# Kernel tuning notes

Hardware: AMD Instinct MI355X
Metric: run time of the kernel (lower is better)

The kernel has to match this reference:

```python
import jax, jax.numpy as jnp
import numpy as np

N = 50000          # nodes
E = 800000         # edges (before self-loops)
F_IN = 128         # num_features
HID = 16           # hidden_dim (per head)
HEADS = 4
NG = 128           # number of graphs in batch
NC = 10            # num_classes
LAYERS = 3
NEG_SLOPE = 0.2    # PyG GATConv default
EPS = 1e-16


def setup_inputs() -> dict:
    key = jax.random.key(0)
    ks = jax.random.split(key, 4 + 4 * LAYERS + 2)
    inp = {}
    inp["x"] = jax.random.normal(ks[0], (N, F_IN), jnp.float32)
    inp["edge_index"] = jax.random.randint(ks[1], (2, E), 0, N, dtype=jnp.int32)
    inp["batch"] = jnp.sort(jax.random.randint(ks[2], (N,), 0, NG, dtype=jnp.int32))
    in_dims = [F_IN] + [HID * HEADS] * (LAYERS - 1)
    for i in range(LAYERS):
        kb = 3 + 4 * i
        s = 1.0 / np.sqrt(in_dims[i])
        inp[f"W{i}"] = jax.random.normal(ks[kb], (in_dims[i], HEADS * HID), jnp.float32) * s
        inp[f"b{i}"] = jnp.zeros((HEADS * HID,), jnp.float32)
        inp[f"as{i}"] = jax.random.normal(ks[kb + 1], (HEADS, HID), jnp.float32) * 0.1
        inp[f"ad{i}"] = jax.random.normal(ks[kb + 2], (HEADS, HID), jnp.float32) * 0.1
    inp["Wr"] = jax.random.normal(ks[3 + 4 * LAYERS], (HEADS * HID, NC), jnp.float32) * (1.0 / np.sqrt(HEADS * HID))
    inp["br"] = jnp.zeros((NC,), jnp.float32)
    return inp


def _gat_layer(x, src, dst, W, b, att_src, att_dst):
    n = x.shape[0]
    h = (x @ W).reshape(n, HEADS, HID)                # [N,H,D]
    a_src = jnp.einsum('nhd,hd->nh', h, att_src)      # [N,H]
    a_dst = jnp.einsum('nhd,hd->nh', h, att_dst)
    logits = jax.nn.leaky_relu(a_src[src] + a_dst[dst], NEG_SLOPE)  # [E,H]
    # segment softmax over destination node
    m = jax.ops.segment_max(logits, dst, num_segments=n)
    e = jnp.exp(logits - m[dst])
    s = jax.ops.segment_sum(e, dst, num_segments=n)
    alpha = e / (s[dst] + EPS)                        # [E,H]
    msg = h[src] * alpha[:, :, None]                  # [E,H,D]
    out = jax.ops.segment_sum(msg, dst, num_segments=n)
    return out.reshape(n, HEADS * HID) + b


def reference(x, edge_index, batch,
              W0, b0, as0, ad0,
              W1, b1, as1, ad1,
              W2, b2, as2, ad2,
              Wr, br):
    # add self loops (PyG GATConv default add_self_loops=True)
    loop = jnp.arange(N, dtype=edge_index.dtype)
    src = jnp.concatenate([edge_index[0], loop])
    dst = jnp.concatenate([edge_index[1], loop])
    params = [(W0, b0, as0, ad0), (W1, b1, as1, ad1), (W2, b2, as2, ad2)]
    h = x
    for (W, b, a_s, a_d) in params:
        h = _gat_layer(h, src, dst, W, b, a_s, a_d)
        h = jax.nn.silu(h)
        # dropout p=0.0 (eval): identity
    pooled = jax.ops.segment_sum(h, batch, num_segments=NG)   # [NG, H*D]
    logits = jax.nn.relu(pooled @ Wr + br)                    # make_mlp ends with ReLU
    return jax.nn.log_softmax(logits, axis=1)
```

## Files before the change

kernel.cpp:

```cpp
#include <hip/hip_runtime.h>
#include <hip/hip_fp16.h>
#include <cstdint>
#include <cstddef>

#define HEADS 4
#define HID 16
#define HD 64
#define NCLS 10
#define NGRAPH 128
#define NEG_SLOPE 0.2f
#define SM_EPS 1e-16f
#define SLOTS 64

static inline size_t alignup(size_t x) { return (x + 255) & ~size_t(255); }

__device__ __forceinline__ unsigned short f2h(float f) {
    __half h = __float2half(f);
    return *reinterpret_cast<unsigned short*>(&h);
}

__global__ void scatter_kernel(const int* __restrict__ srcA, const int* __restrict__ dstA,
                               int E, int npg, int* __restrict__ cursor,
                               unsigned short* __restrict__ csr_src) {
    int g = blockIdx.x & 7;
    int c = blockIdx.x >> 3;
    int nchunks = gridDim.x >> 3;
    int chunk = (E + nchunks - 1) / nchunks;
    int start = c * chunk;
    int end = min(E, start + chunk);
    int lo = g * npg, hi = lo + npg;
    for (int e = start + threadIdx.x; e < end; e += blockDim.x) {
        int d = dstA[e];
        if (d >= lo && d < hi) {
            int pos = atomicAdd(&cursor[d], 1);
            if (pos < SLOTS) csr_src[(size_t)d * SLOTS + pos] = (unsigned short)srcA[e];
        }
    }
}


__global__ __launch_bounds__(256) void gemm_attn_kernel(
        const float* __restrict__ in, const float* __restrict__ Wp,
        const float* __restrict__ as_, const float* __restrict__ ad_,
        unsigned short* __restrict__ hb, float* __restrict__ asrc,
        float* __restrict__ adst, int N, int K) {
    __shared__ __align__(16) float xs[64][68];
    __shared__ __align__(16) float Ws[64][64];
    __shared__ float avl[HD], adl[HD];
    int tid = threadIdx.x, lane = tid & 63, wave = tid >> 6;
    int cg = lane & 15;
    int c0 = cg * 4;
    int r0 = wave * 16 + (lane >> 4) * 4;
    if (tid < HD) { avl[tid] = as_[tid]; adl[tid] = ad_[tid]; }

    int base = blockIdx.x * 64;
    float acc[4][4];
#pragma unroll
    for (int i = 0; i < 4; i++)
#pragma unroll
        for (int j = 0; j < 4; j++) acc[i][j] = 0.f;

    for (int kh = 0; kh < K; kh += 64) {
        __syncthreads();
        for (int i = tid; i < 1024; i += 256) {
            int r = i >> 4, c = (i & 15) * 4;
            float4 v = make_float4(0.f, 0.f, 0.f, 0.f);
            if (base + r < N) v = *(const float4*)(in + (size_t)(base + r) * K + kh + c);
            *(float4*)&xs[r][c] = v;
        }
        for (int i = tid; i < 1024; i += 256) {
            int r = i >> 4, c = (i & 15) * 4;
            *(float4*)&Ws[r][c] = *(const float4*)(Wp + (size_t)(kh + r) * HD + c);
        }
        __syncthreads();

#pragma unroll 8
        for (int k = 0; k < 64; k += 4) {
            float4 wv[4], xv[4];
#pragma unroll
            for (int j = 0; j < 4; j++) wv[j] = *(const float4*)&Ws[k + j][c0];
#pragma unroll
            for (int i = 0; i < 4; i++) xv[i] = *(const float4*)&xs[r0 + i][k];
#pragma unroll
            for (int i = 0; i < 4; i++) {
                acc[i][0] += xv[i].x * wv[0].x + xv[i].y * wv[1].x + xv[i].z * wv[2].x + xv[i].w * wv[3].x;
                acc[i][1] += xv[i].x * wv[0].y + xv[i].y * wv[1].y + xv[i].z * wv[2].y + xv[i].w * wv[3].y;
                acc[i][2] += xv[i].x * wv[0].z + xv[i].y * wv[1].z + xv[i].z * wv[2].z + xv[i].w * wv[3].z;
                acc[i][3] += xv[i].x * wv[0].w + xv[i].y * wv[1].w + xv[i].z * wv[2].w + xv[i].w * wv[3].w;
            }
        }
    }

    int head = cg >> 2;
#pragma unroll
    for (int i = 0; i < 4; i++) {
        int node = base + r0 + i;
        float s = acc[i][0] * avl[c0] + acc[i][1] * avl[c0 + 1] +
                  acc[i][2] * avl[c0 + 2] + acc[i][3] * avl[c0 + 3];
        float d = acc[i][0] * adl[c0] + acc[i][1] * adl[c0 + 1] +
                  acc[i][2] * adl[c0 + 2] + acc[i][3] * adl[c0 + 3];
        s += __shfl_xor(s, 1); s += __shfl_xor(s, 2);
        d += __shfl_xor(d, 1); d += __shfl_xor(d, 2);
        if (node < N) {
            ushort4 pk;
            pk.x = f2h(acc[i][0]); pk.y = f2h(acc[i][1]);
            pk.z = f2h(acc[i][2]); pk.w = f2h(acc[i][3]);
            *(ushort4*)&hb[(size_t)node * HD + c0] = pk;
            if ((cg & 3) == 0) {
                asrc[node * HEADS + head] = s;
                adst[node * HEADS + head] = d;
            }
        }
    }
}

__global__ void gat_gather_kernel(const int* __restrict__ deg,
                                  const unsigned short* __restrict__ csr_src,
                                  int N, const unsigned short* __restrict__ hb,
                                  const float* __restrict__ asrc, const float* __restrict__ adst,
                                  const float* __restrict__ bias, float* __restrict__ out) {
    int wid = (int)((blockIdx.x * (long long)blockDim.x + threadIdx.x) >> 6);
    if (wid >= N) return;
    int lane = threadIdx.x & 63;
    int hh = lane & 3;
    int eg = lane >> 2;
    int e2 = lane >> 5;
    int cp = lane & 31;
    int headc = cp >> 3;

    int beg = wid * SLOTS;
    int cnt = min(deg[wid], SLOTS);
    int end = beg + cnt;

    float4 as4 = *(const float4*)&asrc[wid * 4];
    float4 ad4 = *(const float4*)&adst[wid * 4];
    float l0 = as4.x + ad4.x; l0 = l0 > 0.f ? l0 : NEG_SLOPE * l0;
    float l1 = as4.y + ad4.y; l1 = l1 > 0.f ? l1 : NEG_SLOPE * l1;
    float l2 = as4.z + ad4.z; l2 = l2 > 0.f ? l2 : NEG_SLOPE * l2;
    float l3 = as4.w + ad4.w; l3 = l3 > 0.f ? l3 : NEG_SLOPE * l3;
    float lS_hh = (hh == 0) ? l0 : (hh == 1) ? l1 : (hh == 2) ? l2 : l3;
    float ad_hh = (hh == 0) ? ad4.x : (hh == 1) ? ad4.y : (hh == 2) ? ad4.z : ad4.w;

    float dsum = 0.f;

    float2 acc2 = make_float2(0.f, 0.f);
    if (e2 == 0) {
        __half2 hw = *(const __half2*)&hb[(unsigned)(wid * HD + 2 * cp)];
        acc2.x = __half2float(hw.x);
        acc2.y = __half2float(hw.y);
    }

    for (int c = beg; c < end; c += 16) {
        int e_idx = c + eg;
        unsigned pk = (unsigned)wid << 16;
        float w = 0.f;
        if (e_idx < end) {
            int s = (int)csr_src[e_idx];
            float l = asrc[(unsigned)(s * HEADS + hh)] + ad_hh;
            l = (l > 0.f) ? l : NEG_SLOPE * l;
            w = __expf(l - lS_hh);
            pk = ((unsigned)s << 16) | ((__float_as_uint(w) + 0x8000u) >> 16);
        }
        dsum += w;

        unsigned pp[8];
        __half2 hw[8];
#pragma unroll
        for (int j = 0; j < 8; j++) pp[j] = (unsigned)__shfl((int)pk, (e2 * 8 + j) * 4 + headc);
#pragma unroll
        for (int j = 0; j < 8; j++)
            hw[j] = *(const __half2*)&hb[(pp[j] >> 16) * HD + 2 * cp];
#pragma unroll
        for (int j = 0; j < 8; j++) {
            float wj = __uint_as_float(pp[j] << 16);
            acc2.x += wj * __half2float(hw[j].x);
            acc2.y += wj * __half2float(hw[j].y);
        }
    }

    acc2.x += __shfl_xor(acc2.x, 32);
    acc2.y += __shfl_xor(acc2.y, 32);

    dsum += __shfl_xor(dsum, 4);
    dsum += __shfl_xor(dsum, 8);
    dsum += __shfl_xor(dsum, 16);
    dsum += __shfl_xor(dsum, 32);
    float ssum = __shfl(dsum, headc) + 1.0f;

    if (e2 == 0) {
        float2 bb2 = *(const float2*)&bias[2 * cp];
        float vx = acc2.x / (ssum + SM_EPS) + bb2.x;
        float vy = acc2.y / (ssum + SM_EPS) + bb2.y;
        float2 o;
        o.x = vx / (1.f + expf(-vx));
        o.y = vy / (1.f + expf(-vy));
        *(float2*)&out[(size_t)wid * HD + 2 * cp] = o;
    }
}

__global__ __launch_bounds__(256) void pool_head_kernel(
        const float* __restrict__ h, const int* __restrict__ batch, int N,
        const float* __restrict__ Wr, const float* __restrict__ br,
        float* __restrict__ out) {
    int g = blockIdx.x;
    int tid = threadIdx.x, lane = tid & 63, wv = tid >> 6;

    int a = 0, b = N;
    while (a < b) { int m = (a + b) >> 1; if (batch[m] < g) a = m + 1; else b = m; }
    int lo = a;
    b = N;
    while (a < b) { int m = (a + b) >> 1; if (batch[m] < g + 1) a = m + 1; else b = m; }
    int hi = a;

    float acc = 0.f;
    for (int n = lo + wv; n < hi; n += 4)
        acc += h[(size_t)n * HD + lane];

    __shared__ float sd[4][64];
    sd[wv][lane] = acc;
    __syncthreads();
    if (wv != 0) return;

    float pooled = sd[0][lane] + sd[1][lane] + sd[2][lane] + sd[3][lane];

    float l[NCLS];
    float mx = 0.f;
#pragma unroll
    for (int c = 0; c < NCLS; c++) {
        float p = pooled * Wr[lane * NCLS + c];
#pragma unroll
        for (int off = 1; off < 64; off <<= 1) p += __shfl_xor(p, off);
        p += br[c];
        p = (p > 0.f) ? p : 0.f;
        l[c] = p;
        mx = fmaxf(mx, p);
    }
    float se = 0.f;
#pragma unroll
    for (int c = 0; c < NCLS; c++) se += __expf(l[c] - mx);
    float lse = __logf(se);
    if (lane < NCLS) out[(size_t)g * NCLS + lane] = l[lane] - mx - lse;
}

extern "C" void kernel_launch(void* const* d_in, const int* in_sizes, int n_in,
                              void* d_out, int out_size, void* d_ws, size_t ws_size,
                              hipStream_t stream) {
    const float* x = (const float*)d_in[0];
    const int* ei = (const int*)d_in[1];
    const int* batch = (const int*)d_in[2];
    const float* W[3]  = {(const float*)d_in[3], (const float*)d_in[7],  (const float*)d_in[11]};
    const float* bb[3] = {(const float*)d_in[4], (const float*)d_in[8],  (const float*)d_in[12]};
    const float* as_[3] = {(const float*)d_in[5], (const float*)d_in[9], (const float*)d_in[13]};
    const float* ad_[3] = {(const float*)d_in[6], (const float*)d_in[10], (const float*)d_in[14]};
    const float* Wr = (const float*)d_in[15];
    const float* br = (const float*)d_in[16];

    const int N = in_sizes[2];
    const int E = in_sizes[1] / 2;
    const int F0 = in_sizes[0] / N;

    char* p = (char*)d_ws;
    unsigned short* hb = (unsigned short*)p; p += alignup((size_t)N * HD * 2);
    float* hbuf  = (float*)p; p += alignup((size_t)N * HD * 4);
    float* asrc  = (float*)p; p += alignup((size_t)N * HEADS * 4);
    float* adst  = (float*)p; p += alignup((size_t)N * HEADS * 4);
    int* cursor  = (int*)p;   p += alignup((size_t)N * 4);
    unsigned short* csr_src = (unsigned short*)p; p += alignup((size_t)N * SLOTS * 2);

    const int* srcA = ei;
    const int* dstA = ei + E;

    int ntiles = (N + 63) / 64;
    int npg = (N + 7) / 8;
    int gather_blocks = (int)(((long long)N * 64 + 255) / 256);

    hipMemsetAsync(cursor, 0, (size_t)N * 4, stream);
    scatter_kernel<<<2048, 256, 0, stream>>>(srcA, dstA, E, npg, cursor, csr_src);

    for (int layer = 0; layer < 3; layer++) {
        const float* in = (layer == 0) ? x : hbuf;
        int K = (layer == 0) ? F0 : HD;
        gemm_attn_kernel<<<ntiles, 256, 0, stream>>>(in, W[layer], as_[layer], ad_[layer],
                                                     hb, asrc, adst, N, K);
        gat_gather_kernel<<<gather_blocks, 256, 0, stream>>>(cursor, csr_src, N, hb,
                                                             asrc, adst, bb[layer], hbuf);
    }

    pool_head_kernel<<<NGRAPH, 256, 0, stream>>>(hbuf, batch, N, Wr, br, (float*)d_out);
}
```

Baseline: 232.0 us.

## Use bf16 MFMA for projection GEMM and store activations as bf16

Replaces the scalar fp32 FMA GEMM with bf16 MFMA 16x16x32 instructions, with the input tile and transposed weights held in LDS as bf16 and K fixed per template instantiation. The features h and the inter-layer activations are stored as bf16 instead of fp16 and fp32, which halves the bytes the next layer's GEMM and the pooling kernel read. This trades numerical precision (bf16 mantissa is shorter than fp16's) for less memory traffic and matrix-core throughput. The epilogue now does more shuffles and writes narrow 2-byte scalar stores.

Measured after the change: 228.6 us, median of 2. About the same (-1.5%).

```diff
diff --git a/kernel.cpp b/kernel.cpp
--- a/kernel.cpp
+++ b/kernel.cpp
@@ -1,5 +1,4 @@
 #include <hip/hip_runtime.h>
-#include <hip/hip_fp16.h>
 #include <cstdint>
 #include <cstddef>
 
@@ -14,9 +13,12 @@
 
 static inline size_t alignup(size_t x) { return (x + 255) & ~size_t(255); }
 
-__device__ __forceinline__ unsigned short f2h(float f) {
-    __half h = __float2half(f);
-    return *reinterpret_cast<unsigned short*>(&h);
+typedef short short8 __attribute__((ext_vector_type(8)));
+typedef float f32x4 __attribute__((ext_vector_type(4)));
+typedef unsigned short ushort8 __attribute__((ext_vector_type(8)));
+
+__device__ __forceinline__ unsigned short f2bf(float f) {
+    return (unsigned short)((__float_as_uint(f) + 0x8000u) >> 16);
 }
 
 __global__ void scatter_kernel(const int* __restrict__ srcA, const int* __restrict__ dstA,
@@ -38,77 +40,86 @@
     }
 }
 
-
+template <int K, bool INF32>
 __global__ __launch_bounds__(256) void gemm_attn_kernel(
-        const float* __restrict__ in, const float* __restrict__ Wp,
+        const void* __restrict__ inp, const float* __restrict__ Wp,
         const float* __restrict__ as_, const float* __restrict__ ad_,
         unsigned short* __restrict__ hb, float* __restrict__ asrc,
-        float* __restrict__ adst, int N, int K) {
-    __shared__ __align__(16) float xs[64][68];
-    __shared__ __align__(16) float Ws[64][64];
+        float* __restrict__ adst, int N) {
+    constexpr int KP = K + 8;
+    __shared__ __align__(16) unsigned short xs[64 * KP];
+    __shared__ __align__(16) unsigned short wt[64 * KP];
     __shared__ float avl[HD], adl[HD];
     int tid = threadIdx.x, lane = tid & 63, wave = tid >> 6;
-    int cg = lane & 15;
-    int c0 = cg * 4;
-    int r0 = wave * 16 + (lane >> 4) * 4;
     if (tid < HD) { avl[tid] = as_[tid]; adl[tid] = ad_[tid]; }
-
     int base = blockIdx.x * 64;
-    float acc[4][4];
-#pragma unroll
-    for (int i = 0; i < 4; i++)
-#pragma unroll
-        for (int j = 0; j < 4; j++) acc[i][j] = 0.f;
-
-    for (int kh = 0; kh < K; kh += 64) {
-        __syncthreads();
-        for (int i = tid; i < 1024; i += 256) {
-            int r = i >> 4, c = (i & 15) * 4;
+
+    if (INF32) {
+        const float* in = (const float*)inp;
+        for (int i = tid; i < 64 * K / 4; i += 256) {
+            int flat = i * 4;
+            int r = flat / K, c = flat - r * K;
             float4 v = make_float4(0.f, 0.f, 0.f, 0.f);
-            if (base + r < N) v = *(const float4*)(in + (size_t)(base + r) * K + kh + c);
-            *(float4*)&xs[r][c] = v;
-        }
-        for (int i = tid; i < 1024; i += 256) {
-            int r = i >> 4, c = (i & 15) * 4;
-            *(float4*)&Ws[r][c] = *(const float4*)(Wp + (size_t)(kh + r) * HD + c);
-        }
-        __syncthreads();
-
-#pragma unroll 8
-        for (int k = 0; k < 64; k += 4) {
-            float4 wv[4], xv[4];
-#pragma unroll
-            for (int j = 0; j < 4; j++) wv[j] = *(const float4*)&Ws[k + j][c0];
-#pragma unroll
-            for (int i = 0; i < 4; i++) xv[i] = *(const float4*)&xs[r0 + i][k];
-#pragma unroll
-            for (int i = 0; i < 4; i++) {
-                acc[i][0] += xv[i].x * wv[0].x + xv[i].y * wv[1].x + xv[i].z * wv[2].x + xv[i].w * wv[3].x;
-                acc[i][1] += xv[i].x * wv[0].y + xv[i].y * wv[1].y + xv[i].z * wv[2].y + xv[i].w * wv[3].y;
-                acc[i][2] += xv[i].x * wv[0].z + xv[i].y * wv[1].z + xv[i].z * wv[2].z + xv[i].w * wv[3].z;
-                acc[i][3] += xv[i].x * wv[0].w + xv[i].y * wv[1].w + xv[i].z * wv[2].w + xv[i].w * wv[3].w;
-            }
-        }
-    }
-
-    int head = cg >> 2;
-#pragma unroll
-    for (int i = 0; i < 4; i++) {
-        int node = base + r0 + i;
-        float s = acc[i][0] * avl[c0] + acc[i][1] * avl[c0 + 1] +
-                  acc[i][2] * avl[c0 + 2] + acc[i][3] * avl[c0 + 3];
-        float d = acc[i][0] * adl[c0] + acc[i][1] * adl[c0 + 1] +
-                  acc[i][2] * adl[c0 + 2] + acc[i][3] * adl[c0 + 3];
-        s += __shfl_xor(s, 1); s += __shfl_xor(s, 2);
-        d += __shfl_xor(d, 1); d += __shfl_xor(d, 2);
-        if (node < N) {
-            ushort4 pk;
-            pk.x = f2h(acc[i][0]); pk.y = f2h(acc[i][1]);
-            pk.z = f2h(acc[i][2]); pk.w = f2h(acc[i][3]);
-            *(ushort4*)&hb[(size_t)node * HD + c0] = pk;
-            if ((cg & 3) == 0) {
-                asrc[node * HEADS + head] = s;
-                adst[node * HEADS + head] = d;
+            if (base + r < N) v = *(const float4*)(in + (size_t)(base + r) * K + c);
+            ushort4 u;
+            u.x = f2bf(v.x); u.y = f2bf(v.y); u.z = f2bf(v.z); u.w = f2bf(v.w);
+            *(ushort4*)&xs[r * KP + c] = u;
+        }
+    } else {
+        const unsigned short* in = (const unsigned short*)inp;
+        for (int i = tid; i < 64 * K / 8; i += 256) {
+            int flat = i * 8;
+            int r = flat / K, c = flat - r * K;
+            ushort8 v = (ushort8)(0);
+            if (base + r < N) v = *(const ushort8*)(in + (size_t)(base + r) * K + c);
+            *(ushort8*)&xs[r * KP + c] = v;
+        }
+    }
+    for (int i = tid; i < 64 * K / 4; i += 256) {
+        int flat = i * 4;
+        int r = flat >> 6, c = flat & 63;
+        float4 v = *(const float4*)(Wp + (size_t)r * HD + c);
+        wt[(c + 0) * KP + r] = f2bf(v.x);
+        wt[(c + 1) * KP + r] = f2bf(v.y);
+        wt[(c + 2) * KP + r] = f2bf(v.z);
+        wt[(c + 3) * KP + r] = f2bf(v.w);
+    }
+    __syncthreads();
+
+    int m = lane & 15, kg = lane >> 4;
+    f32x4 acc[4];
+#pragma unroll
+    for (int ct = 0; ct < 4; ct++) acc[ct] = (f32x4){0.f, 0.f, 0.f, 0.f};
+
+    const unsigned short* xrow = &xs[(wave * 16 + m) * KP + kg * 8];
+#pragma unroll
+    for (int kb = 0; kb < K / 32; kb++) {
+        short8 a = *(const short8*)(xrow + kb * 32);
+#pragma unroll
+        for (int ct = 0; ct < 4; ct++) {
+            short8 b = *(const short8*)&wt[(ct * 16 + m) * KP + kb * 32 + kg * 8];
+            acc[ct] = __builtin_amdgcn_mfma_f32_16x16x32_bf16(a, b, acc[ct], 0, 0, 0);
+        }
+    }
+
+#pragma unroll
+    for (int ct = 0; ct < 4; ct++) {
+#pragma unroll
+        for (int j = 0; j < 4; j++) {
+            int node = base + wave * 16 + kg * 4 + j;
+            float hv = acc[ct][j];
+            float s = hv * avl[ct * 16 + m];
+            float d = hv * adl[ct * 16 + m];
+            s += __shfl_xor(s, 1); s += __shfl_xor(s, 2);
+            s += __shfl_xor(s, 4); s += __shfl_xor(s, 8);
+            d += __shfl_xor(d, 1); d += __shfl_xor(d, 2);
+            d += __shfl_xor(d, 4); d += __shfl_xor(d, 8);
+            if (node < N) {
+                hb[(size_t)node * HD + ct * 16 + m] = f2bf(hv);
+                if (m == 0) {
+                    asrc[node * HEADS + ct] = s;
+                    adst[node * HEADS + ct] = d;
+                }
             }
         }
     }
@@ -118,7 +129,7 @@
                                   const unsigned short* __restrict__ csr_src,
                                   int N, const unsigned short* __restrict__ hb,
                                   const float* __restrict__ asrc, const float* __restrict__ adst,
-                                  const float* __restrict__ bias, float* __restrict__ out) {
+                                  const float* __restrict__ bias, unsigned short* __restrict__ outb) {
     int wid = (int)((blockIdx.x * (long long)blockDim.x + threadIdx.x) >> 6);
     if (wid >= N) return;
     int lane = threadIdx.x & 63;
@@ -145,9 +156,9 @@
 
     float2 acc2 = make_float2(0.f, 0.f);
     if (e2 == 0) {
-        __half2 hw = *(const __half2*)&hb[(unsigned)(wid * HD + 2 * cp)];
-        acc2.x = __half2float(hw.x);
-        acc2.y = __half2float(hw.y);
+        unsigned hw = *(const unsigned*)&hb[(unsigned)(wid * HD + 2 * cp)];
+        acc2.x = __uint_as_float(hw << 16);
+        acc2.y = __uint_as_float(hw & 0xffff0000u);
     }
 
     for (int c = beg; c < end; c += 16) {
@@ -163,18 +174,17 @@
         }
         dsum += w;
 
-        unsigned pp[8];
-        __half2 hw[8];
+        unsigned pp[8], hw[8];
 #pragma unroll
         for (int j = 0; j < 8; j++) pp[j] = (unsigned)__shfl((int)pk, (e2 * 8 + j) * 4 + headc);
 #pragma unroll
         for (int j = 0; j < 8; j++)
-            hw[j] = *(const __half2*)&hb[(pp[j] >> 16) * HD + 2 * cp];
+            hw[j] = *(const unsigned*)&hb[(pp[j] >> 16) * HD + 2 * cp];
 #pragma unroll
         for (int j = 0; j < 8; j++) {
             float wj = __uint_as_float(pp[j] << 16);
-            acc2.x += wj * __half2float(hw[j].x);
-            acc2.y += wj * __half2float(hw[j].y);
+            acc2.x += wj * __uint_as_float(hw[j] << 16);
+            acc2.y += wj * __uint_as_float(hw[j] & 0xffff0000u);
         }
     }
 
@@ -191,15 +201,15 @@
         float2 bb2 = *(const float2*)&bias[2 * cp];
         float vx = acc2.x / (ssum + SM_EPS) + bb2.x;
         float vy = acc2.y / (ssum + SM_EPS) + bb2.y;
-        float2 o;
-        o.x = vx / (1.f + expf(-vx));
-        o.y = vy / (1.f + expf(-vy));
-        *(float2*)&out[(size_t)wid * HD + 2 * cp] = o;
+        float ox = vx / (1.f + expf(-vx));
+        float oy = vy / (1.f + expf(-vy));
+        unsigned o = (unsigned)f2bf(ox) | ((unsigned)f2bf(oy) << 16);
+        *(unsigned*)&outb[(size_t)wid * HD + 2 * cp] = o;
     }
 }
 
 __global__ __launch_bounds__(256) void pool_head_kernel(
-        const float* __restrict__ h, const int* __restrict__ batch, int N,
+        const unsigned short* __restrict__ hx, const int* __restrict__ batch, int N,
         const float* __restrict__ Wr, const float* __restrict__ br,
         float* __restrict__ out) {
     int g = blockIdx.x;
@@ -214,7 +224,7 @@
 
     float acc = 0.f;
     for (int n = lo + wv; n < hi; n += 4)
-        acc += h[(size_t)n * HD + lane];
+        acc += __uint_as_float((unsigned)hx[(size_t)n * HD + lane] << 16);
 
     __shared__ float sd[4][64];
     sd[wv][lane] = acc;
@@ -257,11 +267,10 @@
 
     const int N = in_sizes[2];
     const int E = in_sizes[1] / 2;
-    const int F0 = in_sizes[0] / N;
 
     char* p = (char*)d_ws;
     unsigned short* hb = (unsigned short*)p; p += alignup((size_t)N * HD * 2);
-    float* hbuf  = (float*)p; p += alignup((size_t)N * HD * 4);
+    unsigned short* hx = (unsigned short*)p; p += alignup((size_t)N * HD * 2);
     float* asrc  = (float*)p; p += alignup((size_t)N * HEADS * 4);
     float* adst  = (float*)p; p += alignup((size_t)N * HEADS * 4);
     int* cursor  = (int*)p;   p += alignup((size_t)N * 4);
@@ -277,14 +286,16 @@
     hipMemsetAsync(cursor, 0, (size_t)N * 4, stream);
     scatter_kernel<<<2048, 256, 0, stream>>>(srcA, dstA, E, npg, cursor, csr_src);
 
-    for (int layer = 0; layer < 3; layer++) {
-        const float* in = (layer == 0) ? x : hbuf;
-        int K = (layer == 0) ? F0 : HD;
-        gemm_attn_kernel<<<ntiles, 256, 0, stream>>>(in, W[layer], as_[layer], ad_[layer],
-                                                     hb, asrc, adst, N, K);
+    gemm_attn_kernel<128, true><<<ntiles, 256, 0, stream>>>(x, W[0], as_[0], ad_[0],
+                                                            hb, asrc, adst, N);
+    gat_gather_kernel<<<gather_blocks, 256, 0, stream>>>(cursor, csr_src, N, hb,
+                                                         asrc, adst, bb[0], hx);
+    for (int layer = 1; layer < 3; layer++) {
+        gemm_attn_kernel<64, false><<<ntiles, 256, 0, stream>>>(hx, W[layer], as_[layer],
+                                                                ad_[layer], hb, asrc, adst, N);
         gat_gather_kernel<<<gather_blocks, 256, 0, stream>>>(cursor, csr_src, N, hb,
-                                                             asrc, adst, bb[layer], hbuf);
-    }
-
-    pool_head_kernel<<<NGRAPH, 256, 0, stream>>>(hbuf, batch, N, Wr, br, (float*)d_out);
-}
+                                                             asrc, adst, bb[layer], hx);
+    }
+
+    pool_head_kernel<<<NGRAPH, 256, 0, stream>>>(hx, batch, N, Wr, br, (float*)d_out);
+}
```
